# Performance work log

Measured on AMD Instinct MI355X. Metric: run time of the kernel, lower is better.

## Reference

```python
import jax, jax.numpy as jnp
import numpy as np
import math

B, S, D, H = 2, 2048, 1024, 16
HD = D // H            # head dim = 64
E, K = 8, 2            # routed experts, top-k
HM = 1024              # moe_inter_dim (multiple_of=256 keeps it)
HS = 1024              # shared expert hidden = moe_inter_dim * n_shared_experts
EPS = 1e-6
TEMP = 1.0


def setup_inputs() -> dict:
    key = jax.random.key(0)
    ks = jax.random.split(key, 16)
    s = 0.02
    x = jax.random.normal(ks[0], (B, S, D), jnp.float32)
    # RoPE angles: theta = 10000
    inv_freq = 1.0 / (10000.0 ** (np.arange(0, HD, 2, dtype=np.float32) / HD))  # (HD//2,)
    ang = np.arange(S, dtype=np.float32)[:, None] * inv_freq[None, :]           # (S, HD//2)
    freqs_cos = jnp.asarray(np.cos(ang))
    freqs_sin = jnp.asarray(np.sin(ang))
    return {
        "x": x,
        "freqs_cos": freqs_cos,
        "freqs_sin": freqs_sin,
        "att_norm_w": jnp.ones((D,), jnp.float32),
        "ffn_norm_w": jnp.ones((D,), jnp.float32),
        "wq": jax.random.normal(ks[1], (D, D), jnp.float32) * s,
        "wk": jax.random.normal(ks[2], (D, D), jnp.float32) * s,
        "wv": jax.random.normal(ks[3], (D, D), jnp.float32) * s,
        "wo": jax.random.normal(ks[4], (D, D), jnp.float32) * s,
        "gate_w": jax.random.normal(ks[5], (E, D), jnp.float32) * s,
        "ew1": jax.random.normal(ks[6], (E, D, HM), jnp.float32) * s,
        "ew2": jax.random.normal(ks[7], (E, HM, D), jnp.float32) * s,
        "ew3": jax.random.normal(ks[8], (E, D, HM), jnp.float32) * s,
        "sw1": jax.random.normal(ks[9], (D, HS), jnp.float32) * s,
        "sw2": jax.random.normal(ks[10], (HS, D), jnp.float32) * s,
        "sw3": jax.random.normal(ks[11], (D, HS), jnp.float32) * s,
    }


def _rmsnorm(x, w):
    return x * jax.lax.rsqrt(jnp.mean(x * x, axis=-1, keepdims=True) + EPS) * w


def _rope(t, cos, sin):
    # t: (B,H,S,HD); rotate pairs (even, odd) like complex multiply
    tr = t.reshape(B, H, S, HD // 2, 2)
    t0, t1 = tr[..., 0], tr[..., 1]
    c = cos[None, None, :, :]
    s_ = sin[None, None, :, :]
    o0 = t0 * c - t1 * s_
    o1 = t0 * s_ + t1 * c
    return jnp.stack([o0, o1], axis=-1).reshape(B, H, S, HD)


def reference(x, freqs_cos, freqs_sin, att_norm_w, ffn_norm_w,
              wq, wk, wv, wo, gate_w, ew1, ew2, ew3, sw1, sw2, sw3):
    # ---- attention sub-block ----
    xn = _rmsnorm(x, att_norm_w)
    q = (xn @ wq).reshape(B, S, H, HD).transpose(0, 2, 1, 3)  # (B,H,S,HD)
    k = (xn @ wk).reshape(B, S, H, HD).transpose(0, 2, 1, 3)
    v = (xn @ wv).reshape(B, S, H, HD).transpose(0, 2, 1, 3)
    q = _rope(q, freqs_cos, freqs_sin)
    k = _rope(k, freqs_cos, freqs_sin)
    scores = jnp.einsum('bhqd,bhkd->bhqk', q, k) / math.sqrt(HD)
    attn = jax.nn.softmax(scores, axis=-1)
    out = jnp.einsum('bhqk,bhkd->bhqd', attn, v)
    out = out.transpose(0, 2, 1, 3).reshape(B, S, D) @ wo
    h = x + out

    # ---- MoE sub-block ----
    xf = _rmsnorm(h, ffn_norm_w).reshape(-1, D)  # (N,D), N=B*S
    # shared expert (SwiGLU)
    shared = (jax.nn.silu(xf @ sw1) * (xf @ sw3)) @ sw2
    # gate (eval mode: no noise)
    g_scores = (xf @ gate_w.T) / TEMP
    probs = jax.nn.softmax(g_scores, axis=-1)          # (N,E)
    vals, idx = jax.lax.top_k(probs, K)                 # (N,K)
    vals = vals / (jnp.sum(vals, axis=-1, keepdims=True) + 1e-9)
    # per-token per-expert weight (equivalent to scatter into expert_mask)
    mask = jnp.sum(jax.nn.one_hot(idx, E, dtype=xf.dtype) * vals[..., None], axis=1)  # (N,E)
    # routed experts: dense per-expert SwiGLU, weighted combine (zero weight => no contribution)
    h1 = jax.nn.silu(jnp.einsum('nd,edh->enh', xf, ew1)) * jnp.einsum('nd,edh->enh', xf, ew3)
    eo = jnp.einsum('enh,ehd->end', h1, ew2)            # (E,N,D)
    y = jnp.einsum('end,ne->nd', eo, mask) + shared
    return h + y.reshape(B, S, D)
```

## Files before the change

kernel.cpp:

```cpp
#include <hip/hip_runtime.h>
#include <hip/hip_bf16.h>
#include <stdint.h>


typedef __hip_bfloat16 bf16;
typedef __attribute__((ext_vector_type(8))) __bf16 bf16x8;
typedef __attribute__((ext_vector_type(4))) float f32x4;
typedef __attribute__((ext_vector_type(2))) unsigned int u32x2;

#define S_  2048
#define D_  1024
#define N_  4096

__device__ __forceinline__ float b2f(bf16 h) { return __bfloat162float(h); }
__device__ __forceinline__ bf16  f2b(float f) { return __float2bfloat16(f); }

__device__ __forceinline__ bf16x8 ld_bf16x8(const bf16* p) {
    union { uint4 u; bf16x8 v; } x;
    x.u = *(const uint4*)p;
    return x.v;
}

__device__ __forceinline__ void gload_lds16(const void* gsrc, void* ldst) {
    __builtin_amdgcn_global_load_lds(
        (__attribute__((address_space(1))) void*)const_cast<void*>(gsrc),
        (__attribute__((address_space(3))) void*)ldst, 16, 0, 0);
}

__device__ __forceinline__ u32x2 tr16_read(unsigned lds_off) {
    u32x2 d;
    asm volatile("ds_read_b64_tr_b16 %0, %1" : "=v"(d) : "v"(lds_off));
    return d;
}

__global__ __launch_bounds__(256)
void transpose_all(const float* __restrict__ wq, const float* __restrict__ wk,
                   const float* __restrict__ wv, const float* __restrict__ wo,
                   const float* __restrict__ ew1, const float* __restrict__ ew2,
                   const float* __restrict__ ew3, const float* __restrict__ sw1,
                   const float* __restrict__ sw2, const float* __restrict__ sw3,
                   bf16* __restrict__ wqkv_t, bf16* __restrict__ wo_t,
                   bf16* __restrict__ ew13_t, bf16* __restrict__ ew2_t)
{
    __shared__ float t[32][33];
    const int z = blockIdx.z;
    const float* in; bf16* out; int rm = 1, ro = 0;
    if (z < 3)        { in = (z == 0 ? wq : z == 1 ? wk : wv); out = wqkv_t + (size_t)z * 1048576; }
    else if (z == 3)  { in = wo; out = wo_t; }
    else if (z < 12)  { const int e = z - 4;  in = ew1 + (size_t)e * 1048576; out = ew13_t + (size_t)e * 2097152; rm = 2; ro = 0; }
    else if (z < 20)  { const int e = z - 12; in = ew3 + (size_t)e * 1048576; out = ew13_t + (size_t)e * 2097152; rm = 2; ro = 1; }
    else if (z < 28)  { const int e = z - 20; in = ew2 + (size_t)e * 1048576; out = ew2_t + (size_t)e * 1048576; }
    else if (z == 28) { in = sw1; out = ew13_t + (size_t)8 * 2097152; rm = 2; ro = 0; }
    else if (z == 29) { in = sw3; out = ew13_t + (size_t)8 * 2097152; rm = 2; ro = 1; }
    else              { in = sw2; out = ew2_t + (size_t)8 * 1048576; }

    const int c0 = blockIdx.x * 32, r0 = blockIdx.y * 32;
    const int tx = threadIdx.x & 31, ty = threadIdx.x >> 5;
#pragma unroll
    for (int i = 0; i < 32; i += 8)
        t[ty + i][tx] = in[(size_t)(r0 + ty + i) * 1024 + c0 + tx];
    __syncthreads();
#pragma unroll
    for (int i = 0; i < 32; i += 8)
        out[(size_t)((c0 + ty + i) * rm + ro) * 1024 + r0 + tx] = f2b(t[tx][ty + i]);
}

__global__ __launch_bounds__(256)
void rmsnorm_kernel(const float* __restrict__ x, const float* __restrict__ w,
                    bf16* __restrict__ out)
{
    const int n = blockIdx.x;
    const int tid = threadIdx.x;
    const float4 v = *(const float4*)(x + (size_t)n * D_ + tid * 4);
    float ss = v.x * v.x + v.y * v.y + v.z * v.z + v.w * v.w;
#pragma unroll
    for (int m = 1; m < 64; m <<= 1) ss += __shfl_xor(ss, m);
    __shared__ float red[4];
    if ((tid & 63) == 0) red[tid >> 6] = ss;
    __syncthreads();
    const float tot = red[0] + red[1] + red[2] + red[3];
    const float rstd = rsqrtf(tot * (1.0f / D_) + 1e-6f);
    const float4 wv = *(const float4*)(w + tid * 4);
    union { bf16 h[4]; uint2 u; } pk;
    pk.h[0] = f2b(v.x * rstd * wv.x);
    pk.h[1] = f2b(v.y * rstd * wv.y);
    pk.h[2] = f2b(v.z * rstd * wv.z);
    pk.h[3] = f2b(v.w * rstd * wv.w);
    *(uint2*)(out + (size_t)n * D_ + tid * 4) = pk.u;
}

template<int EPI, int MODE>
__global__ __launch_bounds__(256)
void gemm_bt(const bf16* __restrict__ A, const bf16* __restrict__ Bt,
             void* __restrict__ Cout, const float* __restrict__ resid,
             int M, int Kdim, int lda, int ldb, int ldc, long bstride,
             const int* __restrict__ tlist, const int* __restrict__ offs,
             const float* __restrict__ fc, const float* __restrict__ fs)
{
    __shared__ bf16 As[2][128 * 32];
    __shared__ bf16 Bs[2][128 * 32];
    const int tid = threadIdx.x;
    const int wave = tid >> 6, lane = tid & 63;

    int bx, by;
    if constexpr (MODE == 0) {
        const int gx = gridDim.x;
        const int nwg = gx * gridDim.y;
        int flat = blockIdx.y * gx + blockIdx.x;
        flat = (flat & 7) * (nwg >> 3) + (flat >> 3);
        bx = flat % gx; by = flat / gx;
    } else {
        bx = blockIdx.x; by = blockIdx.y;
    }

    int mcount = M, outBase = 0;
    const bf16* Bp = Bt;
    if (MODE != 0) {
        const int e = blockIdx.z;
        outBase = offs[e];
        mcount = offs[e + 1] - outBase;
        Bp = Bt + (size_t)e * bstride;
    }
    const int m0 = by * 128;
    if (m0 >= mcount) return;
    const int n0 = bx * 128;

    const int srow = tid >> 2;
    const int sc4 = tid & 3;
    const int scol = (sc4 ^ (srow & 3)) * 8;
    const bf16* aptr[2];
    const bf16* bptr[2];
#pragma unroll
    for (int i = 0; i < 2; i++) {
        int r = m0 + i * 64 + srow;
        if (r >= mcount) r = mcount - 1;
        long arow;
        if (MODE == 1)      arow = tlist[outBase + r];
        else if (MODE == 2) arow = (long)outBase + r;
        else                arow = r;
        aptr[i] = A + (size_t)arow * lda + scol;
        bptr[i] = Bp + (size_t)(n0 + i * 64 + srow) * ldb + scol;
    }

    f32x4 zero4 = {0.f, 0.f, 0.f, 0.f};
    f32x4 acc[4][4];
#pragma unroll
    for (int m = 0; m < 4; m++)
#pragma unroll
        for (int n = 0; n < 4; n++) acc[m][n] = zero4;

    const int wm = (wave >> 1) * 64, wn = (wave & 1) * 64;
    const int fr = lane & 15, fk = (lane >> 4) * 8;
    const int fks = fk ^ ((fr & 3) << 3);
    const int aoff = (wm + fr) * 32 + fks;
    const int boff = (wn + fr) * 32 + fks;

    const int nkt = Kdim >> 5;
#pragma unroll
    for (int i = 0; i < 2; i++) {
        gload_lds16(aptr[i], (char*)&As[0][0] + i * 4096 + wave * 1024);
        gload_lds16(bptr[i], (char*)&Bs[0][0] + i * 4096 + wave * 1024);
    }

    int p = 0;
    for (int kt = 0; kt < nkt; kt++) {
        if (kt + 1 < nkt) {
            const int ko = (kt + 1) << 5;
#pragma unroll
            for (int i = 0; i < 2; i++) {
                gload_lds16(aptr[i] + ko, (char*)&As[p ^ 1][0] + i * 4096 + wave * 1024);
                gload_lds16(bptr[i] + ko, (char*)&Bs[p ^ 1][0] + i * 4096 + wave * 1024);
            }
            asm volatile("s_waitcnt vmcnt(4)" ::: "memory");
        } else {
            asm volatile("s_waitcnt vmcnt(0)" ::: "memory");
        }
        asm volatile("s_barrier" ::: "memory");

        const bf16* Ab = &As[p][0];
        const bf16* Bb = &Bs[p][0];
        bf16x8 af[4], bfr[4];
#pragma unroll
        for (int m = 0; m < 4; m++) af[m] = ld_bf16x8(&Ab[aoff + m * 512]);
#pragma unroll
        for (int n = 0; n < 4; n++) bfr[n] = ld_bf16x8(&Bb[boff + n * 512]);
#pragma unroll
        for (int m = 0; m < 4; m++)
#pragma unroll
            for (int n = 0; n < 4; n++)
                acc[m][n] = __builtin_amdgcn_mfma_f32_16x16x32_bf16(af[m], bfr[n], acc[m][n], 0, 0, 0);

        asm volatile("s_barrier" ::: "memory");
        p ^= 1;
    }

    const int crow = m0 + wm + (lane >> 4) * 4;
    const int ccol = n0 + wn + fr;
#pragma unroll
    for (int m = 0; m < 4; m++)
#pragma unroll
        for (int n = 0; n < 4; n++)
#pragma unroll
            for (int j = 0; j < 4; j++) {
                const int r = crow + m * 16 + j;
                const int c = ccol + n * 16;
                const float v = acc[m][n][j];
                if (EPI == 3) {
                    const float other = __shfl_xor(v, 1);
                    const float res = (v / (1.f + __expf(-v))) * other;
                    if (((lane & 1) == 0) && r < mcount)
                        ((bf16*)Cout)[(size_t)(outBase + r) * ldc + (c >> 1)] = f2b(res);
                } else if (EPI == 4) {
                    const float other = __shfl_xor(v, 1);
                    float o = v;
                    if (c < 2048) {
                        const int s = r & (S_ - 1);
                        const int jf = (c & 63) >> 1;
                        const float co = fc[s * 32 + jf], si = fs[s * 32 + jf];
                        o = v * co + other * ((c & 1) ? si : -si);
                        if (c < 1024) o *= 0.125f;
                    }
                    ((bf16*)Cout)[(size_t)r * ldc + c] = f2b(o);
                } else if (r < mcount) {
                    const size_t oi = (size_t)(outBase + r) * ldc + c;
                    if (EPI == 0)      ((bf16*)Cout)[oi] = f2b(v);
                    else if (EPI == 1) ((float*)Cout)[oi] = v;
                    else               ((float*)Cout)[oi] = resid[oi] + v;
                }
            }
}

__global__ __launch_bounds__(256)
void attn_kernel(const bf16* __restrict__ qkv, bf16* __restrict__ out)
{
    __shared__ __align__(16) bf16 Ks[64 * 72];
    __shared__ __align__(16) bf16 Vs[4 * 1032 + 8];
    const int tid = threadIdx.x, wave = tid >> 6, lane = tid & 63;
    const int b = blockIdx.z, hh = blockIdx.y;
    const int q0 = blockIdx.x * 128;
    const bf16* base  = qkv + ((size_t)b * S_) * 3072 + (size_t)hh * 64;
    const bf16* kbase = base + 1024;
    const bf16* vbase = base + 2048;
    const int fr = lane & 15, fg = lane >> 4;

    bf16x8 aq[2][2];
#pragma unroll
    for (int qb = 0; qb < 2; qb++)
#pragma unroll
        for (int s2 = 0; s2 < 2; s2++)
            aq[qb][s2] = ld_bf16x8(base + (size_t)(q0 + wave * 32 + qb * 16 + fr) * 3072 + s2 * 32 + fg * 8);

    f32x4 zero4 = {0.f, 0.f, 0.f, 0.f};
    f32x4 acc_o[2][4];
    float mrow[2], lrow[2];
#pragma unroll
    for (int qb = 0; qb < 2; qb++) {
#pragma unroll
        for (int hf = 0; hf < 4; hf++) acc_o[qb][hf] = zero4;
        mrow[qb] = -1e30f; lrow[qb] = 0.f;
    }

    const int srow = tid >> 2, sc4 = tid & 3;
    const unsigned vtr0 =
        (unsigned)(uintptr_t)(__attribute__((address_space(3))) void*)&Vs[0] + lane * 8;

    uint4 kg0, kg1, vg0, vg1;
    {
        const bf16* kr = kbase + (size_t)srow * 3072 + sc4 * 16;
        kg0 = *(const uint4*)kr; kg1 = *(const uint4*)(kr + 8);
        const bf16* vr = vbase + (size_t)srow * 3072 + sc4 * 16;
        vg0 = *(const uint4*)vr; vg1 = *(const uint4*)(vr + 8);
    }

    for (int kv0 = 0; kv0 < S_; kv0 += 64) {
        __syncthreads();
        *(uint4*)&Ks[srow * 72 + sc4 * 16]         = kg0;
        *(uint4*)&Ks[srow * 72 + sc4 * 16 + 8]     = kg1;
        *(uint4*)&Vs[sc4 * 1032 + srow * 16]       = vg0;
        *(uint4*)&Vs[sc4 * 1032 + srow * 16 + 8]   = vg1;
        __syncthreads();
        if (kv0 + 64 < S_) {
            const bf16* kr = kbase + (size_t)(kv0 + 64 + srow) * 3072 + sc4 * 16;
            kg0 = *(const uint4*)kr; kg1 = *(const uint4*)(kr + 8);
            const bf16* vr = vbase + (size_t)(kv0 + 64 + srow) * 3072 + sc4 * 16;
            vg0 = *(const uint4*)vr; vg1 = *(const uint4*)(vr + 8);
        }

        f32x4 sc[4][2];
#pragma unroll
        for (int kt = 0; kt < 4; kt++)
#pragma unroll
            for (int qb = 0; qb < 2; qb++) sc[kt][qb] = zero4;
        __builtin_amdgcn_s_setprio(1);
#pragma unroll
        for (int kt = 0; kt < 4; kt++) {
            const bf16x8 k0 = ld_bf16x8(&Ks[(kt * 16 + fr) * 72 + fg * 8]);
            const bf16x8 k1 = ld_bf16x8(&Ks[(kt * 16 + fr) * 72 + 32 + fg * 8]);
#pragma unroll
            for (int qb = 0; qb < 2; qb++) {
                sc[kt][qb] = __builtin_amdgcn_mfma_f32_16x16x32_bf16(k0, aq[qb][0], sc[kt][qb], 0, 0, 0);
                sc[kt][qb] = __builtin_amdgcn_mfma_f32_16x16x32_bf16(k1, aq[qb][1], sc[kt][qb], 0, 0, 0);
            }
        }
        __builtin_amdgcn_s_setprio(0);

        bf16x8 pcomb[2][2];
        float scalv[2];
#pragma unroll
        for (int qb = 0; qb < 2; qb++) {
            float pm = -1e30f;
#pragma unroll
            for (int kt = 0; kt < 4; kt++)
#pragma unroll
                for (int j = 0; j < 4; j++) pm = fmaxf(pm, sc[kt][qb][j]);
            pm = fmaxf(pm, __shfl_xor(pm, 16));
            pm = fmaxf(pm, __shfl_xor(pm, 32));
            const float mnew = fmaxf(mrow[qb], pm);
            const float scal = __expf(mrow[qb] - mnew);
            mrow[qb] = mnew;
            float ps = 0.f;
            union { bf16 h[16]; bf16x8 v8[2]; } pk;
#pragma unroll
            for (int kt = 0; kt < 4; kt++)
#pragma unroll
                for (int j = 0; j < 4; j++) {
                    const float p = __expf(sc[kt][qb][j] - mnew);
                    ps += p;
                    pk.h[kt * 4 + j] = f2b(p);
                }
            pcomb[qb][0] = pk.v8[0];
            pcomb[qb][1] = pk.v8[1];
            ps += __shfl_xor(ps, 16);
            ps += __shfl_xor(ps, 32);
            lrow[qb] = lrow[qb] * scal + ps;
            scalv[qb] = scal;
        }

#pragma unroll
        for (int j = 0; j < 4; j++) {
            const int src = (lane & 48) + fg * 4 + j;
            const float s0 = __shfl(scalv[0], src);
            const float s1 = __shfl(scalv[1], src);
#pragma unroll
            for (int hf = 0; hf < 4; hf++) {
                acc_o[0][hf][j] *= s0;
                acc_o[1][hf][j] *= s1;
            }
        }

#pragma unroll
        for (int tp = 0; tp < 2; tp++) {
            union { u32x2 d2[2]; bf16x8 v8; } vc[4];
#pragma unroll
            for (int hf = 0; hf < 4; hf++) {
                vc[hf].d2[0] = tr16_read(vtr0 + hf * 2064 + (tp * 2)     * 512);
                vc[hf].d2[1] = tr16_read(vtr0 + hf * 2064 + (tp * 2 + 1) * 512);
            }
            asm volatile("s_waitcnt lgkmcnt(0)" ::: "memory");
            __builtin_amdgcn_sched_barrier(0);
            __builtin_amdgcn_s_setprio(1);
#pragma unroll
            for (int hf = 0; hf < 4; hf++)
#pragma unroll
                for (int qb = 0; qb < 2; qb++)
                    acc_o[qb][hf] = __builtin_amdgcn_mfma_f32_16x16x32_bf16(
                        pcomb[qb][tp], vc[hf].v8, acc_o[qb][hf], 0, 0, 0);
            __builtin_amdgcn_s_setprio(0);
        }
    }

#pragma unroll
    for (int qb = 0; qb < 2; qb++) {
        const float inv = 1.f / lrow[qb];
#pragma unroll
        for (int j = 0; j < 4; j++) {
            const float ij = __shfl(inv, (lane & 48) + fg * 4 + j);
            const int r = q0 + wave * 32 + qb * 16 + fg * 4 + j;
#pragma unroll
            for (int hf = 0; hf < 4; hf++)
                out[((size_t)(b * S_ + r)) * D_ + hh * 64 + hf * 16 + fr] =
                    f2b(acc_o[qb][hf][j] * ij);
        }
    }
}

__global__ __launch_bounds__(256)
void gating_kernel(const float* __restrict__ h, const float* __restrict__ gw,
                   const float* __restrict__ wnorm,
                   int* __restrict__ top_idx, float* __restrict__ top_w)
{
    const int wave = threadIdx.x >> 6, lane = threadIdx.x & 63;
    const int n = blockIdx.x * 4 + wave;
    const float* hr = h + (size_t)n * D_;
    float acc[8] = {0.f, 0.f, 0.f, 0.f, 0.f, 0.f, 0.f, 0.f};
    float ss = 0.f;
    for (int d = lane * 4; d < D_; d += 256) {
        const float4 hv = *(const float4*)(hr + d);
        const float4 wv = *(const float4*)(wnorm + d);
        ss += hv.x * hv.x + hv.y * hv.y + hv.z * hv.z + hv.w * hv.w;
        const float x0 = hv.x * wv.x, x1 = hv.y * wv.y, x2 = hv.z * wv.z, x3 = hv.w * wv.w;
#pragma unroll
        for (int e2 = 0; e2 < 8; e2++) {
            const float4 gv = *(const float4*)(gw + e2 * D_ + d);
            acc[e2] += x0 * gv.x + x1 * gv.y + x2 * gv.z + x3 * gv.w;
        }
    }
#pragma unroll
    for (int m = 1; m < 64; m <<= 1) {
        ss += __shfl_xor(ss, m);
#pragma unroll
        for (int e2 = 0; e2 < 8; e2++) acc[e2] += __shfl_xor(acc[e2], m);
    }
    if (lane == 0) {
        const float rstd = rsqrtf(ss * (1.0f / D_) + 1e-6f);
        float s[8];
#pragma unroll
        for (int e2 = 0; e2 < 8; e2++) s[e2] = acc[e2] * rstd;
        int e0 = 0;
#pragma unroll
        for (int e2 = 1; e2 < 8; e2++) if (s[e2] > s[e0]) e0 = e2;
        int e1 = (e0 == 0) ? 1 : 0;
#pragma unroll
        for (int e2 = 0; e2 < 8; e2++) if (e2 != e0 && s[e2] > s[e1]) e1 = e2;
        const float mx = s[e0];
        float Z = 0.f;
        float p[8];
#pragma unroll
        for (int e2 = 0; e2 < 8; e2++) { p[e2] = __expf(s[e2] - mx); Z += p[e2]; }
        const float v0 = p[e0] / Z, v1 = p[e1] / Z;
        const float sm = v0 + v1 + 1e-9f;
        top_idx[n * 2] = e0; top_idx[n * 2 + 1] = e1;
        top_w[n * 2] = v0 / sm; top_w[n * 2 + 1] = v1 / sm;
    }
}

__global__ __launch_bounds__(1024)
void route_kernel(const int* __restrict__ top_idx, int* __restrict__ offs,
                  int* __restrict__ token_list, int* __restrict__ tok_pos)
{
    __shared__ int hist[8];
    __shared__ int base[8];
    const int tid = threadIdx.x;
    if (tid < 8) hist[tid] = 0;
    __syncthreads();
    int4 e4a = *(const int4*)(top_idx + tid * 8);
    int4 e4b = *(const int4*)(top_idx + tid * 8 + 4);
    int myidx[8] = {e4a.x, e4a.y, e4a.z, e4a.w, e4b.x, e4b.y, e4b.z, e4b.w};
#pragma unroll
    for (int i = 0; i < 8; i++) atomicAdd(&hist[myidx[i]], 1);
    __syncthreads();
    if (tid == 0) {
        int o = 0;
#pragma unroll
        for (int e = 0; e < 8; e++) { base[e] = o; offs[e] = o; o += hist[e]; }
        offs[8] = o;
        offs[9] = o + N_;
    }
    __syncthreads();
    if (tid < 8) hist[tid] = 0;
    __syncthreads();
#pragma unroll
    for (int i = 0; i < 8; i++) {
        const int entry = tid * 8 + i;
        const int e = myidx[i];
        const int pos = base[e] + atomicAdd(&hist[e], 1);
        token_list[pos] = entry >> 1;
        tok_pos[entry] = pos;
    }
#pragma unroll
    for (int i = 0; i < 4; i++)
        token_list[2 * N_ + tid * 4 + i] = tid * 4 + i;
}

__global__ __launch_bounds__(256)
void combine_kernel(const float* __restrict__ h, const bf16* __restrict__ eo,
                    const int* __restrict__ tok_pos, const float* __restrict__ top_w,
                    float* __restrict__ out)
{
    const int idx = blockIdx.x * 256 + threadIdx.x;
    const int n = idx >> 8;
    const int c = (idx & 255) * 4;
    const float4 hv = *(const float4*)(h + (size_t)n * D_ + c);
    const int p0 = tok_pos[n * 2], p1 = tok_pos[n * 2 + 1];
    const float w0 = top_w[n * 2], w1 = top_w[n * 2 + 1];
    union { uint2 u; bf16 hh[4]; } a0, a1, ash;
    a0.u  = *(const uint2*)(eo + (size_t)p0 * D_ + c);
    a1.u  = *(const uint2*)(eo + (size_t)p1 * D_ + c);
    ash.u = *(const uint2*)(eo + (size_t)(2 * N_ + n) * D_ + c);
    float4 r;
    r.x = hv.x + b2f(ash.hh[0]) + w0 * b2f(a0.hh[0]) + w1 * b2f(a1.hh[0]);
    r.y = hv.y + b2f(ash.hh[1]) + w0 * b2f(a0.hh[1]) + w1 * b2f(a1.hh[1]);
    r.z = hv.z + b2f(ash.hh[2]) + w0 * b2f(a0.hh[2]) + w1 * b2f(a1.hh[2]);
    r.w = hv.w + b2f(ash.hh[3]) + w0 * b2f(a0.hh[3]) + w1 * b2f(a1.hh[3]);
    *(float4*)(out + (size_t)n * D_ + c) = r;
}

extern "C" void kernel_launch(void* const* d_in, const int* in_sizes, int n_in,
                              void* d_out, int out_size, void* d_ws, size_t ws_size,
                              hipStream_t stream)
{
    const float* x   = (const float*)d_in[0];
    const float* fc  = (const float*)d_in[1];
    const float* fs  = (const float*)d_in[2];
    const float* anw = (const float*)d_in[3];
    const float* fnw = (const float*)d_in[4];
    const float* wq  = (const float*)d_in[5];
    const float* wk  = (const float*)d_in[6];
    const float* wv  = (const float*)d_in[7];
    const float* wo  = (const float*)d_in[8];
    const float* gw  = (const float*)d_in[9];
    const float* ew1 = (const float*)d_in[10];
    const float* ew2 = (const float*)d_in[11];
    const float* ew3 = (const float*)d_in[12];
    const float* sw1 = (const float*)d_in[13];
    const float* sw2 = (const float*)d_in[14];
    const float* sw3 = (const float*)d_in[15];

    char* ws = (char*)d_ws;
    bf16*  wqkv_t = (bf16*)(ws + 0);
    bf16*  wo_t   = (bf16*)(ws + 6291456);
    bf16*  ew13_t = (bf16*)(ws + 8388608);
    bf16*  ew2_t  = (bf16*)(ws + 46137344);
    bf16*  xn     = (bf16*)(ws + 65011712);
    bf16*  qkv    = (bf16*)(ws + 73400320);
    bf16*  attn   = (bf16*)(ws + 98566144);
    float* hbuf   = (float*)(ws + 106954752);
    bf16*  eo     = (bf16*)(ws + 123731968);
    char*  misc   = ws + 148897792;
    int*   offs       = (int*)(misc + 0);
    int*   top_idx    = (int*)(misc + 128);
    float* top_w      = (float*)(misc + 128 + 32768);
    int*   token_list = (int*)(misc + 128 + 65536);
    int*   tok_pos    = (int*)(misc + 128 + 131072);

    const dim3 tb(256);
    transpose_all<<<dim3(32, 32, 31), tb, 0, stream>>>(
        wq, wk, wv, wo, ew1, ew2, ew3, sw1, sw2, sw3,
        wqkv_t, wo_t, ew13_t, ew2_t);

    rmsnorm_kernel<<<N_, tb, 0, stream>>>(x, anw, xn);
    gemm_bt<4, 0><<<dim3(24, 32, 1), tb, 0, stream>>>(xn, wqkv_t, qkv, nullptr,
        N_, 1024, 1024, 1024, 3072, 0, nullptr, nullptr, fc, fs);
    attn_kernel<<<dim3(16, 16, 2), tb, 0, stream>>>(qkv, attn);
    gemm_bt<2, 0><<<dim3(8, 32, 1), tb, 0, stream>>>(attn, wo_t, hbuf, x,
        N_, 1024, 1024, 1024, 1024, 0, nullptr, nullptr, nullptr, nullptr);

    rmsnorm_kernel<<<N_, tb, 0, stream>>>(hbuf, fnw, xn);
    gating_kernel<<<N_ / 4, tb, 0, stream>>>(hbuf, gw, fnw, top_idx, top_w);
    route_kernel<<<1, 1024, 0, stream>>>(top_idx, offs, token_list, tok_pos);

    gemm_bt<3, 1><<<dim3(16, 32, 9), tb, 0, stream>>>(xn, ew13_t, qkv, nullptr,
        0, 1024, 1024, 1024, 1024, 2097152, token_list, offs, nullptr, nullptr);
    gemm_bt<0, 2><<<dim3(8, 32, 9), tb, 0, stream>>>((const bf16*)qkv, ew2_t, eo, nullptr,
        0, 1024, 1024, 1024, 1024, 1048576, nullptr, offs, nullptr, nullptr);

    combine_kernel<<<4096, tb, 0, stream>>>(hbuf, eo, tok_pos, top_w, (float*)d_out);
}
```

Measured before the change: 393.0 us.

## Switch GEMM to 32x32x16 MFMA tiles and widen weight transpose tiles

The GEMM inner loop now issues 32x32x16 bf16 MFMAs on 2x2 accumulator tiles per wave instead of 16x16x32 on 4x4 tiles. This means fewer LDS fragment reads and fewer MFMA issues per k-step, and the epilogue indexing is rewritten for the new output layout. The LDS swizzle changes to a new XOR pattern meant to avoid bank conflicts for the 32-row fragment reads. The weight transpose kernel moves to 64x64 tiles with float4 loads and packed 4-wide bf16 stores, cutting per-element memory traffic overhead at the cost of a larger shared buffer.

```diff
diff --git a/kernel.cpp b/kernel.cpp
--- a/kernel.cpp
+++ b/kernel.cpp
@@ -6,6 +6,7 @@
 typedef __hip_bfloat16 bf16;
 typedef __attribute__((ext_vector_type(8))) __bf16 bf16x8;
 typedef __attribute__((ext_vector_type(4))) float f32x4;
+typedef __attribute__((ext_vector_type(16))) float f32x16;
 typedef __attribute__((ext_vector_type(2))) unsigned int u32x2;
 
 #define S_  2048
@@ -32,6 +33,8 @@
     asm volatile("ds_read_b64_tr_b16 %0, %1" : "=v"(d) : "v"(lds_off));
     return d;
 }
+
+__device__ __forceinline__ int swz4(int r) { return ((r >> 1) ^ (r >> 3)) & 3; }
 
 __global__ __launch_bounds__(256)
 void transpose_all(const float* __restrict__ wq, const float* __restrict__ wk,
@@ -42,7 +45,7 @@
                    bf16* __restrict__ wqkv_t, bf16* __restrict__ wo_t,
                    bf16* __restrict__ ew13_t, bf16* __restrict__ ew2_t)
 {
-    __shared__ float t[32][33];
+    __shared__ float t[64][65];
     const int z = blockIdx.z;
     const float* in; bf16* out; int rm = 1, ro = 0;
     if (z < 3)        { in = (z == 0 ? wq : z == 1 ? wk : wv); out = wqkv_t + (size_t)z * 1048576; }
@@ -54,15 +57,20 @@
     else if (z == 29) { in = sw3; out = ew13_t + (size_t)8 * 2097152; rm = 2; ro = 1; }
     else              { in = sw2; out = ew2_t + (size_t)8 * 1048576; }
 
-    const int c0 = blockIdx.x * 32, r0 = blockIdx.y * 32;
-    const int tx = threadIdx.x & 31, ty = threadIdx.x >> 5;
-#pragma unroll
-    for (int i = 0; i < 32; i += 8)
-        t[ty + i][tx] = in[(size_t)(r0 + ty + i) * 1024 + c0 + tx];
+    const int c0 = blockIdx.x * 64, r0 = blockIdx.y * 64;
+    const int tx = (threadIdx.x & 15) * 4, ty = threadIdx.x >> 4;
+#pragma unroll
+    for (int i = 0; i < 4; i++)
+        *(float4*)&t[ty + i * 16][tx] = *(const float4*)(in + (size_t)(r0 + ty + i * 16) * 1024 + c0 + tx);
     __syncthreads();
 #pragma unroll
-    for (int i = 0; i < 32; i += 8)
-        out[(size_t)((c0 + ty + i) * rm + ro) * 1024 + r0 + tx] = f2b(t[tx][ty + i]);
+    for (int i = 0; i < 4; i++) {
+        const int lc = ty + i * 16;
+        union { bf16 h[4]; uint2 u; } pk;
+#pragma unroll
+        for (int j = 0; j < 4; j++) pk.h[j] = f2b(t[tx + j][lc]);
+        *(uint2*)&out[(size_t)((c0 + lc) * rm + ro) * 1024 + r0 + tx] = pk.u;
+    }
 }
 
 __global__ __launch_bounds__(256)
@@ -127,7 +135,7 @@
 
     const int srow = tid >> 2;
     const int sc4 = tid & 3;
-    const int scol = (sc4 ^ (srow & 3)) * 8;
+    const int scol = (sc4 ^ swz4(srow)) * 8;
     const bf16* aptr[2];
     const bf16* bptr[2];
 #pragma unroll
@@ -142,18 +150,29 @@
         bptr[i] = Bp + (size_t)(n0 + i * 64 + srow) * ldb + scol;
     }
 
-    f32x4 zero4 = {0.f, 0.f, 0.f, 0.f};
-    f32x4 acc[4][4];
-#pragma unroll
-    for (int m = 0; m < 4; m++)
-#pragma unroll
-        for (int n = 0; n < 4; n++) acc[m][n] = zero4;
+    f32x16 acc[2][2];
+#pragma unroll
+    for (int tm = 0; tm < 2; tm++)
+#pragma unroll
+        for (int tn = 0; tn < 2; tn++)
+#pragma unroll
+            for (int i = 0; i < 16; i++) acc[tm][tn][i] = 0.f;
 
     const int wm = (wave >> 1) * 64, wn = (wave & 1) * 64;
-    const int fr = lane & 15, fk = (lane >> 4) * 8;
-    const int fks = fk ^ ((fr & 3) << 3);
-    const int aoff = (wm + fr) * 32 + fks;
-    const int boff = (wn + fr) * 32 + fks;
+    const int l31 = lane & 31, l5 = lane >> 5;
+
+    int aoff[2][2], boff[2][2];
+#pragma unroll
+    for (int tm = 0; tm < 2; tm++) {
+        const int ra = wm + tm * 32 + l31;
+        const int rb = wn + tm * 32 + l31;
+#pragma unroll
+        for (int kk = 0; kk < 2; kk++) {
+            const int g = kk * 2 + l5;
+            aoff[tm][kk] = ra * 32 + (g ^ swz4(ra)) * 8;
+            boff[tm][kk] = rb * 32 + (g ^ swz4(rb)) * 8;
+        }
+    }
 
     const int nkt = Kdim >> 5;
 #pragma unroll
@@ -179,32 +198,33 @@
 
         const bf16* Ab = &As[p][0];
         const bf16* Bb = &Bs[p][0];
-        bf16x8 af[4], bfr[4];
-#pragma unroll
-        for (int m = 0; m < 4; m++) af[m] = ld_bf16x8(&Ab[aoff + m * 512]);
-#pragma unroll
-        for (int n = 0; n < 4; n++) bfr[n] = ld_bf16x8(&Bb[boff + n * 512]);
-#pragma unroll
-        for (int m = 0; m < 4; m++)
-#pragma unroll
-            for (int n = 0; n < 4; n++)
-                acc[m][n] = __builtin_amdgcn_mfma_f32_16x16x32_bf16(af[m], bfr[n], acc[m][n], 0, 0, 0);
+#pragma unroll
+        for (int kk = 0; kk < 2; kk++) {
+            bf16x8 af[2], bfr[2];
+#pragma unroll
+            for (int tm = 0; tm < 2; tm++) af[tm] = ld_bf16x8(&Ab[aoff[tm][kk]]);
+#pragma unroll
+            for (int tn = 0; tn < 2; tn++) bfr[tn] = ld_bf16x8(&Bb[boff[tn][kk]]);
+#pragma unroll
+            for (int tm = 0; tm < 2; tm++)
+#pragma unroll
+                for (int tn = 0; tn < 2; tn++)
+                    acc[tm][tn] = __builtin_amdgcn_mfma_f32_32x32x16_bf16(af[tm], bfr[tn], acc[tm][tn], 0, 0, 0);
+        }
 
         asm volatile("s_barrier" ::: "memory");
         p ^= 1;
     }
 
-    const int crow = m0 + wm + (lane >> 4) * 4;
-    const int ccol = n0 + wn + fr;
-#pragma unroll
-    for (int m = 0; m < 4; m++)
-#pragma unroll
-        for (int n = 0; n < 4; n++)
-#pragma unroll
-            for (int j = 0; j < 4; j++) {
-                const int r = crow + m * 16 + j;
-                const int c = ccol + n * 16;
-                const float v = acc[m][n][j];
+#pragma unroll
+    for (int tm = 0; tm < 2; tm++)
+#pragma unroll
+        for (int tn = 0; tn < 2; tn++)
+#pragma unroll
+            for (int i = 0; i < 16; i++) {
+                const int r = m0 + wm + tm * 32 + (i & 3) + 8 * (i >> 2) + 4 * l5;
+                const int c = n0 + wn + tn * 32 + l31;
+                const float v = acc[tm][tn][i];
                 if (EPI == 3) {
                     const float other = __shfl_xor(v, 1);
                     const float res = (v / (1.f + __expf(-v))) * other;
@@ -534,7 +554,7 @@
     int*   tok_pos    = (int*)(misc + 128 + 131072);
 
     const dim3 tb(256);
-    transpose_all<<<dim3(32, 32, 31), tb, 0, stream>>>(
+    transpose_all<<<dim3(16, 16, 31), tb, 0, stream>>>(
         wq, wk, wv, wo, ew1, ew2, ew3, sw1, sw2, sw3,
         wqkv_t, wo_t, ew13_t, ew2_t);
 
```

After: 399.1 us. About the same (+1.6%).
